# Kernel tuning notes

Hardware: AMD Instinct MI355X
Metric: run time of the kernel (lower is better)

## Reference

```python
import jax, jax.numpy as jnp
import numpy as np
from jax import lax

# --- model/problem dims (see init_kwargs) ---
G, NPG, R, F, HID, L = 40, 500, 8, 256, 256, 3   # graphs(frames), nodes/graph, relations, feat, hidden, layers
N = G * NPG                                       # 20000 nodes
EPG = 8000
E = G * EPG                                       # 320000 edges
TOTAL = L * HID                                   # 768 = concat of layer outputs
LSTM_IN, LSTM_HID, NCLASS = 256, 256, 2
RATIO = 0.5
K = int(np.ceil(RATIO * NPG))                     # 250 nodes kept per graph by SAGPool


def setup_inputs() -> dict:
    key = jax.random.key(0)
    ks = jax.random.split(key, 16)
    s = 0.05
    x = jax.random.normal(ks[0], (N, F), dtype=jnp.float32)
    # intra-graph edges: node ids offset by graph index
    off = jnp.arange(G, dtype=jnp.int32)[:, None] * NPG
    src = jax.random.randint(ks[1], (G, EPG), 0, NPG, dtype=jnp.int32) + off
    dst = jax.random.randint(ks[2], (G, EPG), 0, NPG, dtype=jnp.int32) + off
    edge_index = jnp.stack([src.reshape(-1), dst.reshape(-1)])
    edge_attr = jax.random.randint(ks[3], (E,), 0, R, dtype=jnp.int32)
    batch = jnp.repeat(jnp.arange(G, dtype=jnp.int32), NPG)
    # RGCN layer params (layer0 in=F==HID so all layers stack)
    conv_W = jax.random.normal(ks[4], (L, R, HID, HID), dtype=jnp.float32) * s
    conv_root = jax.random.normal(ks[5], (L, HID, HID), dtype=jnp.float32) * s
    conv_bias = jnp.zeros((L, HID), dtype=jnp.float32)
    # SAGPool scorer: RGCNConv(TOTAL, 1, R)
    pool_W = jax.random.normal(ks[6], (R, TOTAL, 1), dtype=jnp.float32) * s
    pool_root = jax.random.normal(ks[7], (TOTAL, 1), dtype=jnp.float32) * s
    pool_bias = jnp.zeros((1,), dtype=jnp.float32)
    fc1_W = jax.random.normal(ks[8], (LSTM_IN, TOTAL), dtype=jnp.float32) * s
    fc1_b = jnp.zeros((LSTM_IN,), dtype=jnp.float32)
    W_ih = jax.random.normal(ks[9], (4 * LSTM_HID, LSTM_IN), dtype=jnp.float32) * s
    W_hh = jax.random.normal(ks[10], (4 * LSTM_HID, LSTM_HID), dtype=jnp.float32) * s
    b_ih = jnp.zeros((4 * LSTM_HID,), dtype=jnp.float32)
    b_hh = jnp.zeros((4 * LSTM_HID,), dtype=jnp.float32)
    fc2_W = jax.random.normal(ks[11], (NCLASS, LSTM_HID), dtype=jnp.float32) * s
    fc2_b = jnp.zeros((NCLASS,), dtype=jnp.float32)
    return dict(x=x, edge_index=edge_index, edge_attr=edge_attr, batch=batch,
                conv_W=conv_W, conv_root=conv_root, conv_bias=conv_bias,
                pool_W=pool_W, pool_root=pool_root, pool_bias=pool_bias,
                fc1_W=fc1_W, fc1_b=fc1_b, W_ih=W_ih, W_hh=W_hh, b_ih=b_ih, b_hh=b_hh,
                fc2_W=fc2_W, fc2_b=fc2_b)


def rgcn_conv(x, src, dst, etype, W, root, bias):
    """PyG (Fast)RGCNConv: per-relation mean aggregation summed over relations + root + bias."""
    num_nodes = x.shape[0]
    Rr = W.shape[0]
    h_all = jnp.einsum('ni,rio->rno', x, W)          # [R, N, out] per-relation transform
    msg = h_all[etype, src]                           # [E, out] per-edge message
    seg = dst * Rr + etype                            # (node, relation) segment id
    cnt = jax.ops.segment_sum(jnp.ones((src.shape[0],), x.dtype), seg,
                              num_segments=num_nodes * Rr)
    norm = 1.0 / jnp.maximum(cnt[seg], 1.0)           # per-(dst,rel) mean normalization
    agg = jax.ops.segment_sum(msg * norm[:, None], dst, num_segments=num_nodes)
    return agg + x @ root + bias


def lstm_scan(xs, W_ih, W_hh, b_ih, b_hh):
    """torch.nn.LSTM (single layer, batch=1) over sequence xs [T, in]; torch gate order i,f,g,o."""
    H = W_hh.shape[1]
    def step(carry, xt):
        h, c = carry
        gates = xt @ W_ih.T + h @ W_hh.T + b_ih + b_hh
        i, f, g, o = jnp.split(gates, 4)
        c = jax.nn.sigmoid(f) * c + jax.nn.sigmoid(i) * jnp.tanh(g)
        h = jax.nn.sigmoid(o) * jnp.tanh(c)
        return (h, c), h
    init = (jnp.zeros((H,), xs.dtype), jnp.zeros((H,), xs.dtype))
    (h, c), ys = lax.scan(step, init, xs)
    return ys, h


def reference(x, edge_index, edge_attr, batch,
              conv_W, conv_root, conv_bias,
              pool_W, pool_root, pool_bias,
              fc1_W, fc1_b, W_ih, W_hh, b_ih, b_hh, fc2_W, fc2_b):
    src, dst = edge_index[0], edge_index[1]
    # stacked RGCN layers, outputs concatenated (dropout omitted: eval mode)
    h = x
    outs = []
    for l in range(L):
        h = jax.nn.relu(rgcn_conv(h, src, dst, edge_attr, conv_W[l], conv_root[l], conv_bias[l]))
        outs.append(h)
    xc = jnp.concatenate(outs, axis=-1)               # [N, TOTAL]
    # SAGPool: RGCN scorer -> tanh -> per-graph top-k (batch is contiguous equal-size graphs)
    score = jnp.tanh(rgcn_conv(xc, src, dst, edge_attr, pool_W, pool_root, pool_bias).reshape(-1))
    topv, topi = lax.top_k(score.reshape(G, NPG), K)  # [G, K]
    xg = xc.reshape(G, NPG, TOTAL)
    xsel = jnp.take_along_axis(xg, topi[:, :, None], axis=1) * topv[:, :, None]
    # readout_type='mean': global_mean_pool over kept nodes per graph
    readout = xsel.mean(axis=1)                       # [G, TOTAL]
    h1 = jax.nn.relu(readout @ fc1_W.T + fc1_b)       # [G, LSTM_IN]
    # temporal_type='lstm_last': last hidden state over the G-frame sequence
    _, hlast = lstm_scan(h1, W_ih, W_hh, b_ih, b_hh)  # [LSTM_HID]
    logits = hlast @ fc2_W.T + fc2_b                  # [NCLASS]
    return jax.nn.log_softmax(logits, axis=-1)
```

## Files before the change

### kernel.cpp

```cpp
#include <hip/hip_runtime.h>

typedef unsigned short u16;
typedef short bf8 __attribute__((ext_vector_type(8)));
typedef short bf4 __attribute__((ext_vector_type(4)));
typedef float f4 __attribute__((ext_vector_type(4)));
typedef _Float16 h2v __attribute__((ext_vector_type(2)));
typedef __fp16 g2v __attribute__((ext_vector_type(2)));
typedef unsigned int u4v __attribute__((ext_vector_type(4)));

#define N_NODES 20000
#define N_EDGES 320000
#define NGRAPH 40
#define NPG 500
#define KTOP 250
#define NSEG (N_NODES * 8)

#define P_CONV_BIAS 0
#define P_POOL_W    768
#define P_POOL_ROOT 6912
#define P_POOL_BIAS 7680
#define P_FC1_W     7688
#define P_FC1_B     204296
#define P_W_IH      204552
#define P_B_IH      466696
#define P_B_HH      467720
#define P_FC2_W     468744
#define P_FC2_B     469256
#define P_TOTAL     469264

__device__ __forceinline__ float b2f(u16 u) {
    union { unsigned int i; float f; } v; v.i = ((unsigned int)u) << 16; return v.f;
}
__device__ __forceinline__ u16 f2b(float f) {
    union { float f; unsigned int i; } v; v.f = f;
    unsigned int x = v.i;
    return (u16)((x + 0x7fffu + ((x >> 16) & 1u)) >> 16);
}
__device__ __forceinline__ float wred(float s) {
    #pragma unroll
    for (int off = 32; off > 0; off >>= 1) s += __shfl_down(s, off);
    return s;
}
__device__ __forceinline__ float fdot2u(unsigned a, unsigned b, float c) {
#if __has_builtin(__builtin_amdgcn_fdot2)
    union { unsigned u; h2v h; } ua, ub; ua.u = a; ub.u = b;
    return __builtin_amdgcn_fdot2(ua.h, ub.h, c, false);
#else
    union { unsigned u; g2v h; } ua, ub; ua.u = a; ub.u = b;
    return c + (float)ua.h[0] * (float)ub.h[0] + (float)ua.h[1] * (float)ub.h[1];
#endif
}
__device__ __forceinline__ unsigned packh2(float a, float b) {
    g2v h = __builtin_amdgcn_cvt_pkrtz(a, b);
    union { g2v h; unsigned u; } v; v.h = h; return v.u;
}
__device__ __forceinline__ float sigm_f(float x) {
    return 1.0f / (1.0f + __expf(-x));
}
__device__ __forceinline__ float tanh_f(float x) {
    return 1.0f - 2.0f / (1.0f + __expf(2.0f * x));
}

__global__ void k_init(unsigned int* __restrict__ flag, unsigned int* __restrict__ cnt,
                       unsigned int* __restrict__ ctr) {
    int i = blockIdx.x * 256 + threadIdx.x;
    if (i < 64) flag[i] = 0u;
    if (i < NSEG) { cnt[i] = 0u; ctr[i] = 0u; }
}

__global__ void k_detect1(const u16* __restrict__ xr, int n, unsigned int* __restrict__ fb) {
    unsigned int local = 0;
    for (int i = blockIdx.x * 256 + threadIdx.x; i < n; i += 64 * 256) {
        unsigned int u = xr[i];
        if (((u >> 7) & 0xFFu) == 0xFFu) local++;
    }
    local = (unsigned int)wred((float)local);
    if ((threadIdx.x & 63) == 0 && local) atomicAdd(&fb[1], local);
}
__global__ void k_detect2(unsigned int* __restrict__ fb) {
    fb[0] = (fb[1] > 8u) ? 1u : 0u;
}

__device__ __forceinline__ u16 load_cvt(const void* src, size_t i, bool f32) {
    return f32 ? f2b(((const float*)src)[i]) : ((const u16*)src)[i];
}

__global__ void k_cvt_all(const void* conv_bias, const void* pool_W, const void* pool_root,
                          const void* pool_bias, const void* fc1_W, const void* fc1_b,
                          const void* W_ih, const void* b_ih, const void* b_hh,
                          const void* fc2_W, const void* fc2_b,
                          u16* __restrict__ parms, const unsigned int* __restrict__ flag) {
    int i = blockIdx.x * 256 + threadIdx.x;
    if (i >= P_TOTAL) return;
    bool f32 = (*flag != 0u);
    u16 v;
    if      (i < P_CONV_BIAS + 768)    v = load_cvt(conv_bias, i - P_CONV_BIAS, f32);
    else if (i < P_POOL_W + 6144)      v = load_cvt(pool_W,    i - P_POOL_W, f32);
    else if (i < P_POOL_ROOT + 768)    v = load_cvt(pool_root, i - P_POOL_ROOT, f32);
    else if (i < P_POOL_BIAS + 1)      v = load_cvt(pool_bias, i - P_POOL_BIAS, f32);
    else if (i < P_FC1_W && i >= P_POOL_BIAS) return;
    else if (i < P_FC1_W + 196608)     v = load_cvt(fc1_W,    i - P_FC1_W, f32);
    else if (i < P_FC1_B + 256)        v = load_cvt(fc1_b,    i - P_FC1_B, f32);
    else if (i < P_W_IH + 262144)      v = load_cvt(W_ih,     i - P_W_IH, f32);
    else if (i < P_B_IH + 1024)        v = load_cvt(b_ih,     i - P_B_IH, f32);
    else if (i < P_B_HH + 1024)        v = load_cvt(b_hh,     i - P_B_HH, f32);
    else if (i < P_FC2_W + 512)        v = load_cvt(fc2_W,    i - P_FC2_W, f32);
    else if (i < P_FC2_B + 2)          v = load_cvt(fc2_b,    i - P_FC2_B, f32);
    else return;
    parms[i] = v;
}

__global__ void k_stage_x(const void* __restrict__ src, u16* __restrict__ xc,
                          const unsigned int* __restrict__ flag) {
    int i = blockIdx.x * 256 + threadIdx.x;
    if (i >= N_NODES * 32) return;
    int n = i >> 5, o = (i & 31) * 8;
    bf8 v;
    if (*flag != 0u) {
        const float* s = (const float*)src + (size_t)n * 256 + o;
        #pragma unroll
        for (int c = 0; c < 8; ++c) v[c] = (short)f2b(s[c]);
    } else {
        v = *(const bf8*)((const u16*)src + (size_t)n * 256 + o);
    }
    *(bf8*)(xc + (size_t)n * 768 + 512 + o) = v;
}

__global__ void k_count(const int* __restrict__ dst, const int* __restrict__ et,
                        unsigned int* __restrict__ cnt) {
    int e = blockIdx.x * 256 + threadIdx.x;
    if (e < N_EDGES) {
        unsigned d = (unsigned)dst[e]; if (d >= N_NODES) d = 0;
        unsigned r = (unsigned)et[e] & 7u;
        atomicAdd(&cnt[d * 8 + r], 1u);
    }
}
__global__ void k_inv(const unsigned int* __restrict__ cnt, float* __restrict__ inv, int n) {
    int i = blockIdx.x * 256 + threadIdx.x;
    if (i < n) {
        unsigned int c = cnt[i];
        inv[i] = 1.0f / (float)(c < 1u ? 1u : c);
    }
}

__global__ void k_scan1(const unsigned int* __restrict__ cnt, unsigned int* __restrict__ seg,
                        unsigned int* __restrict__ bsum) {
    __shared__ unsigned int s[256];
    int t = threadIdx.x, i = blockIdx.x * 256 + t;
    unsigned int v = (i < NSEG) ? cnt[i] : 0u;
    s[t] = v;
    __syncthreads();
    for (int off = 1; off < 256; off <<= 1) {
        unsigned int add = (t >= off) ? s[t - off] : 0u;
        __syncthreads();
        s[t] += add;
        __syncthreads();
    }
    if (i < NSEG) seg[i] = s[t] - v;
    if (t == 255) bsum[blockIdx.x] = s[255];
}
__global__ void k_scan2(unsigned int* __restrict__ bsum, int nb) {
    __shared__ unsigned int s[1024];
    int t = threadIdx.x;
    unsigned int v = (t < nb) ? bsum[t] : 0u;
    s[t] = v;
    __syncthreads();
    for (int off = 1; off < 1024; off <<= 1) {
        unsigned int add = (t >= off) ? s[t - off] : 0u;
        __syncthreads();
        s[t] += add;
        __syncthreads();
    }
    if (t < nb) bsum[t] = s[t] - v;
}
__global__ void k_scan3(unsigned int* __restrict__ seg, const unsigned int* __restrict__ bsum) {
    int i = blockIdx.x * 256 + threadIdx.x;
    if (i < NSEG) seg[i] += bsum[i >> 8];
    if (i == 0) seg[NSEG] = N_EDGES;
}
__global__ void k_place(const int* __restrict__ src, const int* __restrict__ dst,
                        const int* __restrict__ et, const unsigned int* __restrict__ seg,
                        unsigned int* __restrict__ ctr, const float* __restrict__ inv,
                        unsigned int* __restrict__ skey, float* __restrict__ sw, int chn) {
    int e = blockIdx.x * 256 + threadIdx.x;
    if (e >= N_EDGES) return;
    unsigned s = (unsigned)src[e]; if (s >= N_NODES) s = 0;
    unsigned d = (unsigned)dst[e]; if (d >= N_NODES) d = 0;
    unsigned r = (unsigned)et[e] & 7u;
    unsigned key = d * 8 + r;
    unsigned pos = seg[key] + atomicAdd(&ctr[key], 1u);
    unsigned base = (d / (unsigned)chn) * (unsigned)chn;
    unsigned sl = s - base;
    if (sl >= (unsigned)chn) sl = 0u;
    skey[pos] = sl | (r << 16);
    sw[pos] = inv[key];
}

__global__ void k_transpose2(const void* __restrict__ conv_W, const void* __restrict__ conv_root,
                             u16* __restrict__ Wt, const unsigned int* __restrict__ flag) {
    int idx = blockIdx.x * 256 + threadIdx.x;
    if (idx >= 3 * 36 * 256 * 64) return;
    bool f32 = (*flag != 0u);
    int kk = idx & 63;
    int n = (idx >> 6) & 255;
    int lc = idx >> 14;
    int l = lc / 36, ck = lc % 36;
    int k = ck * 64 + kk;
    u16 v;
    if (k < 2048) {
        int r = k >> 8, i = k & 255;
        v = load_cvt(conv_W, ((size_t)((l * 8 + r) * 256 + i)) * 256 + n, f32);
    } else {
        int i = k - 2048;
        v = load_cvt(conv_root, ((size_t)(l * 256 + i)) * 256 + n, f32);
    }
    Wt[idx] = v;
}
__global__ void k_whh4(const void* __restrict__ W_hh, unsigned int* __restrict__ whh4,
                       const unsigned int* __restrict__ flag) {
    int idx = blockIdx.x * 256 + threadIdx.x;
    if (idx >= 32 * 1024 * 4) return;
    int c = idx & 3, j = (idx >> 2) & 1023, i4 = idx >> 12;
    int i2 = i4 * 4 + c;
    bool f32 = (*flag != 0u);
    float a, b;
    if (f32) {
        a = ((const float*)W_hh)[j * 256 + 2 * i2];
        b = ((const float*)W_hh)[j * 256 + 2 * i2 + 1];
    } else {
        a = b2f(((const u16*)W_hh)[j * 256 + 2 * i2]);
        b = b2f(((const u16*)W_hh)[j * 256 + 2 * i2 + 1]);
    }
    whh4[idx] = packh2(a, b);
}

__launch_bounds__(256, 3)
__global__ void k_layer2(const u16* __restrict__ xprev,
                         const u16* __restrict__ WtL,
                         u16* __restrict__ Hall, int n0, int chn) {
    __shared__ u16 As[64 * 264];
    int m0 = n0 + blockIdx.x * 64;
    int rg = blockIdx.y;
    int nend = n0 + chn;
    int wave = threadIdx.x >> 6, lane = threadIdx.x & 63;
    int mrow = lane & 15, quad = lane >> 4;
    int nbase = wave * 64;

    {
        int row = threadIdx.x >> 2, sg = threadIdx.x & 3;
        int gm = m0 + row;
        u16* dstp = As + row * 264 + sg * 64;
        if (gm < nend) {
            const u16* srcp = xprev + (size_t)gm * 768 + sg * 64;
            #pragma unroll
            for (int c = 0; c < 8; ++c)
                *(bf8*)(dstp + c * 8) = *(const bf8*)(srcp + c * 8);
        } else {
            bf8 z = {0, 0, 0, 0, 0, 0, 0, 0};
            #pragma unroll
            for (int c = 0; c < 8; ++c) *(bf8*)(dstp + c * 8) = z;
        }
    }
    __syncthreads();

    f4 acc[4][4];
    #pragma unroll
    for (int nt = 0; nt < 4; ++nt)
        #pragma unroll
        for (int mh = 0; mh < 4; ++mh) acc[nt][mh] = (f4){0.0f, 0.0f, 0.0f, 0.0f};

    const u16* WtR = WtL + (size_t)(rg * 4) * 16384;
    #pragma unroll
    for (int c4 = 0; c4 < 4; ++c4) {
        const u16* Bck = WtR + (size_t)c4 * 16384;
        #pragma unroll
        for (int ks = 0; ks < 2; ++ks) {
            bf8 a[4];
            #pragma unroll
            for (int mh = 0; mh < 4; ++mh)
                a[mh] = *(const bf8*)(As + (mh * 16 + mrow) * 264 + c4 * 64 + ks * 32 + quad * 8);
            #pragma unroll
            for (int nt = 0; nt < 4; ++nt) {
                bf8 b = *(const bf8*)(Bck + (size_t)(nbase + nt * 16 + mrow) * 64
                                      + ks * 32 + quad * 8);
                #pragma unroll
                for (int mh = 0; mh < 4; ++mh)
                    acc[nt][mh] = __builtin_amdgcn_mfma_f32_16x16x32_bf16(a[mh], b, acc[nt][mh], 0, 0, 0);
            }
        }
    }

    __syncthreads();
    #pragma unroll
    for (int nt = 0; nt < 4; ++nt) {
        int col = nbase + nt * 16 + mrow;
        #pragma unroll
        for (int mh = 0; mh < 4; ++mh)
            #pragma unroll
            for (int v = 0; v < 4; ++v)
                As[(mh * 16 + quad * 4 + v) * 264 + col] = f2b(acc[nt][mh][v]);
    }
    __syncthreads();
    {
        int row = threadIdx.x >> 2, sg = threadIdx.x & 3;
        int gm = m0 + row;
        if (gm < nend) {
            u16* dst = Hall + ((size_t)rg * chn + (gm - n0)) * 256 + sg * 64;
            const u16* srcp = As + row * 264 + sg * 64;
            #pragma unroll
            for (int c = 0; c < 8; ++c)
                *(bf8*)(dst + c * 8) = *(const bf8*)(srcp + c * 8);
        }
    }
}

__launch_bounds__(256)
__global__ void k_gather(const unsigned int* __restrict__ seg,
                         const unsigned int* __restrict__ skey,
                         const float* __restrict__ sw,
                         const u16* __restrict__ Hall,
                         const u16* __restrict__ bias,
                         u16* __restrict__ xc, int colbase, int n0, int chn) {
    int nl = blockIdx.x * 4 + (threadIdx.x >> 6);
    int n = n0 + nl;
    int lane = threadIdx.x & 63;
    int c0 = lane * 4;
    unsigned e0 = seg[n * 8], e1 = seg[n * 8 + 8];
    float a0 = 0.0f, a1 = 0.0f, a2 = 0.0f, a3 = 0.0f;
    unsigned key = 0; float w = 0.0f;
    if (e0 < e1) { key = skey[e0]; w = sw[e0]; }
    for (unsigned e = e0; e < e1;) {
        unsigned kc = key; float wc = w;
        ++e;
        if (e < e1) { key = skey[e]; w = sw[e]; }
        const u16* row = Hall + ((size_t)(kc >> 16) * chn + (kc & 0xFFFFu)) * 256 + c0;
        bf4 v = *(const bf4*)row;
        a0 += wc * b2f((u16)v[0]);
        a1 += wc * b2f((u16)v[1]);
        a2 += wc * b2f((u16)v[2]);
        a3 += wc * b2f((u16)v[3]);
    }
    const u16* rr = Hall + ((size_t)8 * chn + nl) * 256 + c0;
    bf4 rv = *(const bf4*)rr;
    float o0 = a0 + b2f((u16)rv[0]) + b2f(bias[c0 + 0]);
    float o1 = a1 + b2f((u16)rv[1]) + b2f(bias[c0 + 1]);
    float o2 = a2 + b2f((u16)rv[2]) + b2f(bias[c0 + 2]);
    float o3 = a3 + b2f((u16)rv[3]) + b2f(bias[c0 + 3]);
    bf4 o;
    o[0] = (short)f2b(o0 > 0.0f ? o0 : 0.0f);
    o[1] = (short)f2b(o1 > 0.0f ? o1 : 0.0f);
    o[2] = (short)f2b(o2 > 0.0f ? o2 : 0.0f);
    o[3] = (short)f2b(o3 > 0.0f ? o3 : 0.0f);
    *(bf4*)(xc + (size_t)n * 768 + colbase + c0) = o;
}

__launch_bounds__(256)
__global__ void k_pool(const u16* __restrict__ xc, const u16* __restrict__ parms,
                       float* __restrict__ p, float* __restrict__ score) {
    int n = blockIdx.x * 4 + (threadIdx.x >> 6);
    if (n >= N_NODES) return;
    int lane = threadIdx.x & 63;
    const u16* xr = xc + (size_t)n * 768;
    float acc[9];
    #pragma unroll
    for (int rr = 0; rr < 9; ++rr) acc[rr] = 0.0f;
    #pragma unroll
    for (int q = 0; q < 12; ++q) {
        int f = lane + 64 * q;
        float xv = b2f(xr[f]);
        #pragma unroll
        for (int rr = 0; rr < 8; ++rr)
            acc[rr] += xv * b2f(parms[P_POOL_W + rr * 768 + f]);
        acc[8] += xv * b2f(parms[P_POOL_ROOT + f]);
    }
    #pragma unroll
    for (int rr = 0; rr < 9; ++rr) acc[rr] = wred(acc[rr]);
    if (lane == 0) {
        #pragma unroll
        for (int rr = 0; rr < 8; ++rr) p[rr * N_NODES + n] = acc[rr];
        score[n] = acc[8] + b2f(parms[P_POOL_BIAS]);
    }
}
__global__ void k_scatter_pool(const int* __restrict__ src, const int* __restrict__ dst,
                               const int* __restrict__ et, const float* __restrict__ inv,
                               const float* __restrict__ p, float* __restrict__ score) {
    int e = blockIdx.x * 256 + threadIdx.x;
    if (e >= N_EDGES) return;
    int r = et[e] & 7;
    unsigned s = (unsigned)src[e]; if (s >= N_NODES) s = 0;
    unsigned d = (unsigned)dst[e]; if (d >= N_NODES) d = 0;
    atomicAdd(&score[d], inv[d * 8 + r] * p[r * N_NODES + s]);
}

__launch_bounds__(256)
__global__ void k_sort(const float* __restrict__ score, unsigned int* __restrict__ topidx,
                       float* __restrict__ topv) {
    __shared__ unsigned long long keys[512];
    __shared__ float vals[512];
    int g = blockIdx.x, tid = threadIdx.x;
    for (int i = tid; i < 512; i += 256) {
        unsigned long long key;
        float v = 0.0f;
        if (i < NPG) {
            v = tanhf(score[g * NPG + i]);
            unsigned int u = __float_as_uint(v);
            u = (u & 0x80000000u) ? ~u : (u | 0x80000000u);
            u = ~u;
            key = ((unsigned long long)u << 32) | (unsigned int)i;
        } else {
            key = 0xFFFFFFFFFFFFFFFFull;
        }
        keys[i] = key;
        vals[i] = v;
    }
    __syncthreads();
    for (int k = 2; k <= 512; k <<= 1)
        for (int j = k >> 1; j > 0; j >>= 1) {
            for (int i = tid; i < 512; i += 256) {
                int ixj = i ^ j;
                if (ixj > i) {
                    bool up = ((i & k) == 0);
                    unsigned long long a = keys[i], b = keys[ixj];
                    if ((a > b) == up) { keys[i] = b; keys[ixj] = a; }
                }
            }
            __syncthreads();
        }
    if (tid < KTOP) {
        int idx = (int)(keys[tid] & 511u);
        topidx[g * 256 + tid] = (unsigned)idx;
        topv[g * 256 + tid] = vals[idx];
    }
}

__launch_bounds__(256)
__global__ void k_readout(const unsigned int* __restrict__ topidx,
                          const float* __restrict__ topv,
                          const u16* __restrict__ xc, float* __restrict__ readout) {
    __shared__ unsigned int sidx[KTOP];
    __shared__ float sv[KTOP];
    __shared__ float part[256];
    int g = blockIdx.x, cb = blockIdx.y;
    int tid = threadIdx.x;
    if (tid < KTOP) { sidx[tid] = topidx[g * 256 + tid]; sv[tid] = topv[g * 256 + tid]; }
    __syncthreads();
    int fl = tid & 63, ng = tid >> 6;
    int f = cb * 64 + fl;
    float acc = 0.0f;
    for (int j = ng; j < KTOP; j += 4)
        acc += sv[j] * b2f(xc[(size_t)(g * NPG + sidx[j]) * 768 + f]);
    part[tid] = acc;
    __syncthreads();
    if (tid < 64) {
        float s = part[tid] + part[64 + tid] + part[128 + tid] + part[192 + tid];
        readout[(size_t)g * 768 + cb * 64 + tid] = s * (1.0f / (float)KTOP);
    }
}

__global__ void k_fc1(const float* __restrict__ readout, const u16* __restrict__ parms,
                      float* __restrict__ h1) {
    int wid = blockIdx.x * 4 + (threadIdx.x >> 6);
    if (wid >= NGRAPH * 256) return;
    int g = wid >> 8, o = wid & 255, lane = threadIdx.x & 63;
    const float* rr = readout + (size_t)g * 768;
    const u16* w = parms + P_FC1_W + (size_t)o * 768;
    float s = 0.0f;
    #pragma unroll
    for (int q = 0; q < 12; ++q) { int f = lane + 64 * q; s += rr[f] * b2f(w[f]); }
    s = wred(s);
    if (lane == 0) { s += b2f(parms[P_FC1_B + o]); h1[g * 256 + o] = s > 0.0f ? s : 0.0f; }
}
__global__ void k_gx(const float* __restrict__ h1, const u16* __restrict__ parms,
                     float* __restrict__ gx) {
    int wid = blockIdx.x * 4 + (threadIdx.x >> 6);
    if (wid >= NGRAPH * 1024) return;
    int t = wid >> 10, j = wid & 1023, lane = threadIdx.x & 63;
    const float* xr = h1 + t * 256;
    const u16* w = parms + P_W_IH + (size_t)j * 256;
    float s = 0.0f;
    #pragma unroll
    for (int q = 0; q < 4; ++q) { int f = lane + 64 * q; s += xr[f] * b2f(w[f]); }
    s = wred(s);
    if (lane == 0) gx[t * 1024 + j] = s + b2f(parms[P_B_IH + j]) + b2f(parms[P_B_HH + j]);
}

__launch_bounds__(512, 1)
__global__ void k_lstm(const float* __restrict__ gx, const unsigned int* __restrict__ whh4,
                       const u16* __restrict__ parms, void* __restrict__ out,
                       const unsigned int* __restrict__ flag) {
    __shared__ float hs[256];
    __shared__ unsigned int hs2[128];
    __shared__ float gs[1024];
    __shared__ float red[2];
    int tid = threadIdx.x;
    int j0 = tid, j1 = tid + 512;
    u4v wa[24], wb[24];
    #pragma unroll
    for (int q = 0; q < 24; ++q) {
        wa[q] = *(const u4v*)(whh4 + (((size_t)q * 1024) + j0) * 4);
        wb[q] = *(const u4v*)(whh4 + (((size_t)q * 1024) + j1) * 4);
    }
    asm volatile("" : "+v"(wa[0]), "+v"(wa[1]), "+v"(wa[2]), "+v"(wa[3]),
                      "+v"(wa[4]), "+v"(wa[5]), "+v"(wa[6]), "+v"(wa[7]),
                      "+v"(wa[8]), "+v"(wa[9]), "+v"(wa[10]), "+v"(wa[11]),
                      "+v"(wa[12]), "+v"(wa[13]), "+v"(wa[14]), "+v"(wa[15]),
                      "+v"(wa[16]), "+v"(wa[17]), "+v"(wa[18]), "+v"(wa[19]),
                      "+v"(wa[20]), "+v"(wa[21]), "+v"(wa[22]), "+v"(wa[23]));
    asm volatile("" : "+v"(wb[0]), "+v"(wb[1]), "+v"(wb[2]), "+v"(wb[3]),
                      "+v"(wb[4]), "+v"(wb[5]), "+v"(wb[6]), "+v"(wb[7]),
                      "+v"(wb[8]), "+v"(wb[9]), "+v"(wb[10]), "+v"(wb[11]),
                      "+v"(wb[12]), "+v"(wb[13]), "+v"(wb[14]), "+v"(wb[15]),
                      "+v"(wb[16]), "+v"(wb[17]), "+v"(wb[18]), "+v"(wb[19]),
                      "+v"(wb[20]), "+v"(wb[21]), "+v"(wb[22]), "+v"(wb[23]));
    if (tid < 256) hs[tid] = 0.0f;
    if (tid < 128) hs2[tid] = 0u;
    float c = 0.0f;
    __syncthreads();
    for (int t = 0; t < NGRAPH; ++t) {
        float g0 = gx[t * 1024 + j0];
        float g1 = gx[t * 1024 + j1];
        #pragma unroll
        for (int q = 0; q < 24; ++q) {
            #pragma unroll
            for (int cc = 0; cc < 4; ++cc) {
                unsigned h2 = hs2[q * 4 + cc];
                g0 = fdot2u(wa[q][cc], h2, g0);
                g1 = fdot2u(wb[q][cc], h2, g1);
            }
        }
        #pragma unroll 2
        for (int q = 24; q < 32; ++q) {
            u4v v0 = *(const u4v*)(whh4 + (((size_t)q * 1024) + j0) * 4);
            u4v v1 = *(const u4v*)(whh4 + (((size_t)q * 1024) + j1) * 4);
            #pragma unroll
            for (int cc = 0; cc < 4; ++cc) {
                unsigned h2 = hs2[q * 4 + cc];
                g0 = fdot2u(v0[cc], h2, g0);
                g1 = fdot2u(v1[cc], h2, g1);
            }
        }
        gs[j0] = g0;
        gs[j1] = g1;
        __syncthreads();
        if (tid < 256) {
            float gi = sigm_f(gs[tid]);
            float gf = sigm_f(gs[256 + tid]);
            float gg = tanh_f(gs[512 + tid]);
            float go = sigm_f(gs[768 + tid]);
            c = gf * c + gi * gg;
            float h = go * tanh_f(c);
            hs[tid] = h;
            float ho = __shfl(h, (tid & 63) ^ 1);
            if (!(tid & 1)) hs2[tid >> 1] = packh2(h, ho);
        }
        __syncthreads();
    }
    if (tid < 128) {
        int cls = tid >> 6, lane = tid & 63;
        float s = 0.0f;
        #pragma unroll
        for (int q = 0; q < 4; ++q) {
            int d = lane + 64 * q;
            s += hs[d] * b2f(parms[P_FC2_W + cls * 256 + d]);
        }
        s = wred(s);
        if (lane == 0) red[cls] = s + b2f(parms[P_FC2_B + cls]);
    }
    __syncthreads();
    if (tid == 0) {
        float l0 = red[0], l1 = red[1];
        float m = fmaxf(l0, l1);
        float lse = m + logf(expf(l0 - m) + expf(l1 - m));
        float o0 = l0 - lse, o1 = l1 - lse;
        if (*flag) { ((float*)out)[0] = o0; ((float*)out)[1] = o1; }
        else       { ((u16*)out)[0] = f2b(o0); ((u16*)out)[1] = f2b(o1); }
    }
}

struct WS {
    unsigned int* flag; unsigned int* cnt; float* inv; unsigned int* seg; unsigned int* ctr;
    unsigned int* skey; float* sw; unsigned int* bsum;
    u16* Wt2; u16* xc; u16* Hall; float* p; float* score;
    unsigned int* topidx; float* topv;
    float* readout; float* h1; float* gx; unsigned int* whh4; u16* parms;
    size_t need;
};
static WS plan(char* base, int chn) {
    WS w; size_t off = 0;
    auto take = [&](size_t bytes) -> char* {
        char* p = base + off; off += (bytes + 255) & ~(size_t)255; return p;
    };
    w.flag    = (unsigned int*)take(256);
    w.cnt     = (unsigned int*)take((size_t)NSEG * 4);
    w.inv     = (float*)take((size_t)NSEG * 4);
    w.seg     = (unsigned int*)take((size_t)(NSEG + 1) * 4);
    w.ctr     = (unsigned int*)take((size_t)NSEG * 4);
    w.skey    = (unsigned int*)take((size_t)N_EDGES * 4);
    w.sw      = (float*)take((size_t)N_EDGES * 4);
    w.bsum    = (unsigned int*)take(1024 * 4);
    w.Wt2     = (u16*)take((size_t)3 * 36 * 256 * 64 * 2);
    w.xc      = (u16*)take((size_t)N_NODES * 768 * 2);
    w.Hall    = (u16*)take((size_t)9 * chn * 256 * 2);
    w.p       = (float*)take((size_t)8 * N_NODES * 4);
    w.score   = (float*)take((size_t)N_NODES * 4);
    w.topidx  = (unsigned int*)take((size_t)NGRAPH * 256 * 4);
    w.topv    = (float*)take((size_t)NGRAPH * 256 * 4);
    w.readout = (float*)take((size_t)NGRAPH * 768 * 4);
    w.h1      = (float*)take((size_t)NGRAPH * 256 * 4);
    w.gx      = (float*)take((size_t)NGRAPH * 1024 * 4);
    w.whh4    = (unsigned int*)take((size_t)32 * 1024 * 4 * 4);
    w.parms   = (u16*)take((size_t)P_TOTAL * 2);
    w.need = off;
    return w;
}

extern "C" void kernel_launch(void* const* d_in, const int* in_sizes, int n_in,
                              void* d_out, int out_size, void* d_ws, size_t ws_size,
                              hipStream_t stream) {
    (void)in_sizes; (void)n_in; (void)out_size;
    const void* x        = d_in[0];
    const int* edge_index= (const int*)d_in[1];
    const int* edge_attr = (const int*)d_in[2];
    const void* conv_W   = d_in[4];
    const void* conv_root= d_in[5];
    const void* conv_bias= d_in[6];
    const void* pool_W   = d_in[7];
    const void* pool_root= d_in[8];
    const void* pool_bias= d_in[9];
    const void* fc1_W    = d_in[10];
    const void* fc1_b    = d_in[11];
    const void* W_ih     = d_in[12];
    const void* W_hh     = d_in[13];
    const void* b_ih     = d_in[14];
    const void* b_hh     = d_in[15];
    const void* fc2_W    = d_in[16];
    const void* fc2_b    = d_in[17];

    const int* e_src = edge_index;
    const int* e_dst = edge_index + N_EDGES;

    if (ws_size == 0) ws_size = (size_t)64 << 20;
    int chn = 500;
    {
        const int ladder[8] = {20000, 10000, 5000, 4000, 2500, 2000, 1000, 500};
        for (int i = 0; i < 8; ++i) {
            if (plan((char*)d_ws, ladder[i]).need <= ws_size) { chn = ladder[i]; break; }
        }
    }
    WS w = plan((char*)d_ws, chn);

    k_init<<<(NSEG + 255) / 256, 256, 0, stream>>>(w.flag, w.cnt, w.ctr);
    k_detect1<<<64, 256, 0, stream>>>((const u16*)x, 1 << 18, w.flag);
    k_detect2<<<1, 1, 0, stream>>>(w.flag);

    k_count<<<1250, 256, 0, stream>>>(e_dst, edge_attr, w.cnt);
    k_inv<<<(NSEG + 255) / 256, 256, 0, stream>>>(w.cnt, w.inv, NSEG);
    k_scan1<<<625, 256, 0, stream>>>(w.cnt, w.seg, w.bsum);
    k_scan2<<<1, 1024, 0, stream>>>(w.bsum, 625);
    k_scan3<<<(NSEG + 255) / 256, 256, 0, stream>>>(w.seg, w.bsum);
    k_place<<<1250, 256, 0, stream>>>(e_src, e_dst, edge_attr, w.seg, w.ctr, w.inv,
                                      w.skey, w.sw, chn);

    k_cvt_all<<<(P_TOTAL + 255) / 256, 256, 0, stream>>>(
        conv_bias, pool_W, pool_root, pool_bias, fc1_W, fc1_b,
        W_ih, b_ih, b_hh, fc2_W, fc2_b, w.parms, w.flag);

    k_stage_x<<<2500, 256, 0, stream>>>(x, w.xc, w.flag);
    k_transpose2<<<6912, 256, 0, stream>>>(conv_W, conv_root, w.Wt2, w.flag);
    k_whh4<<<512, 256, 0, stream>>>(W_hh, w.whh4, w.flag);

    int nch = N_NODES / chn;
    int gx_tiles = (chn + 63) / 64;
    for (int l = 0; l < 3; ++l) {
        const u16* xprev = w.xc + (l == 0 ? 512 : (l - 1) * 256);
        const u16* WtL = w.Wt2 + (size_t)l * 36 * 16384;
        const u16* bias = w.parms + P_CONV_BIAS + l * 256;
        for (int c = 0; c < nch; ++c) {
            int n0 = c * chn;
            k_layer2<<<dim3(gx_tiles, 9), 256, 0, stream>>>(xprev, WtL, w.Hall, n0, chn);
            k_gather<<<chn / 4, 256, 0, stream>>>(w.seg, w.skey, w.sw, w.Hall, bias,
                                                  w.xc, l * 256, n0, chn);
        }
    }

    k_pool<<<5000, 256, 0, stream>>>(w.xc, w.parms, w.p, w.score);
    k_scatter_pool<<<1250, 256, 0, stream>>>(e_src, e_dst, edge_attr, w.inv, w.p, w.score);
    k_sort<<<NGRAPH, 256, 0, stream>>>(w.score, w.topidx, w.topv);
    k_readout<<<dim3(NGRAPH, 12), 256, 0, stream>>>(w.topidx, w.topv, w.xc, w.readout);
    k_fc1<<<2560, 256, 0, stream>>>(w.readout, w.parms, w.h1);
    k_gx<<<10240, 256, 0, stream>>>(w.h1, w.parms, w.gx);
    k_lstm<<<1, 512, 0, stream>>>(w.gx, w.whh4, w.parms, d_out, w.flag);
}
```

Before: 691.6 us.

## Fuse setup and tail kernels, drop inverse-count buffer, allow uneven chunk sizes

Merges the parameter, input, weight-transpose and W_hh packing kernels into a single prep launch. Folds the detect flag finalisation into the edge count kernel, and computes inverse degree counts on the fly instead of materialising them. The sort, readout, fc1 and input-gate projection become one per-graph tail kernel. Chunking now permits a non-divisor cap (7000) with a remainder chunk. Together these cut launch count and intermediate buffers, but the tail now runs serially in only 40 blocks, which may cost more than it saves.

```diff
diff --git a/kernel.cpp b/kernel.cpp
--- a/kernel.cpp
+++ b/kernel.cpp
@@ -28,6 +28,12 @@
 #define P_FC2_B     469256
 #define P_TOTAL     469264
 
+#define PR_A0 0
+#define PR_B0 469264
+#define PR_C0 (PR_B0 + 640000)
+#define PR_D0 (PR_C0 + 1769472)
+#define PR_END (PR_D0 + 131072)
+
 __device__ __forceinline__ float b2f(u16 u) {
     union { unsigned int i; float f; } v; v.i = ((unsigned int)u) << 16; return v.f;
 }
@@ -77,69 +83,19 @@
     local = (unsigned int)wred((float)local);
     if ((threadIdx.x & 63) == 0 && local) atomicAdd(&fb[1], local);
 }
-__global__ void k_detect2(unsigned int* __restrict__ fb) {
-    fb[0] = (fb[1] > 8u) ? 1u : 0u;
-}
 
 __device__ __forceinline__ u16 load_cvt(const void* src, size_t i, bool f32) {
     return f32 ? f2b(((const float*)src)[i]) : ((const u16*)src)[i];
 }
 
-__global__ void k_cvt_all(const void* conv_bias, const void* pool_W, const void* pool_root,
-                          const void* pool_bias, const void* fc1_W, const void* fc1_b,
-                          const void* W_ih, const void* b_ih, const void* b_hh,
-                          const void* fc2_W, const void* fc2_b,
-                          u16* __restrict__ parms, const unsigned int* __restrict__ flag) {
-    int i = blockIdx.x * 256 + threadIdx.x;
-    if (i >= P_TOTAL) return;
-    bool f32 = (*flag != 0u);
-    u16 v;
-    if      (i < P_CONV_BIAS + 768)    v = load_cvt(conv_bias, i - P_CONV_BIAS, f32);
-    else if (i < P_POOL_W + 6144)      v = load_cvt(pool_W,    i - P_POOL_W, f32);
-    else if (i < P_POOL_ROOT + 768)    v = load_cvt(pool_root, i - P_POOL_ROOT, f32);
-    else if (i < P_POOL_BIAS + 1)      v = load_cvt(pool_bias, i - P_POOL_BIAS, f32);
-    else if (i < P_FC1_W && i >= P_POOL_BIAS) return;
-    else if (i < P_FC1_W + 196608)     v = load_cvt(fc1_W,    i - P_FC1_W, f32);
-    else if (i < P_FC1_B + 256)        v = load_cvt(fc1_b,    i - P_FC1_B, f32);
-    else if (i < P_W_IH + 262144)      v = load_cvt(W_ih,     i - P_W_IH, f32);
-    else if (i < P_B_IH + 1024)        v = load_cvt(b_ih,     i - P_B_IH, f32);
-    else if (i < P_B_HH + 1024)        v = load_cvt(b_hh,     i - P_B_HH, f32);
-    else if (i < P_FC2_W + 512)        v = load_cvt(fc2_W,    i - P_FC2_W, f32);
-    else if (i < P_FC2_B + 2)          v = load_cvt(fc2_b,    i - P_FC2_B, f32);
-    else return;
-    parms[i] = v;
-}
-
-__global__ void k_stage_x(const void* __restrict__ src, u16* __restrict__ xc,
-                          const unsigned int* __restrict__ flag) {
-    int i = blockIdx.x * 256 + threadIdx.x;
-    if (i >= N_NODES * 32) return;
-    int n = i >> 5, o = (i & 31) * 8;
-    bf8 v;
-    if (*flag != 0u) {
-        const float* s = (const float*)src + (size_t)n * 256 + o;
-        #pragma unroll
-        for (int c = 0; c < 8; ++c) v[c] = (short)f2b(s[c]);
-    } else {
-        v = *(const bf8*)((const u16*)src + (size_t)n * 256 + o);
-    }
-    *(bf8*)(xc + (size_t)n * 768 + 512 + o) = v;
-}
-
 __global__ void k_count(const int* __restrict__ dst, const int* __restrict__ et,
-                        unsigned int* __restrict__ cnt) {
+                        unsigned int* __restrict__ cnt, unsigned int* __restrict__ fb) {
     int e = blockIdx.x * 256 + threadIdx.x;
+    if (e == 0) fb[0] = (fb[1] > 8u) ? 1u : 0u;
     if (e < N_EDGES) {
         unsigned d = (unsigned)dst[e]; if (d >= N_NODES) d = 0;
         unsigned r = (unsigned)et[e] & 7u;
         atomicAdd(&cnt[d * 8 + r], 1u);
-    }
-}
-__global__ void k_inv(const unsigned int* __restrict__ cnt, float* __restrict__ inv, int n) {
-    int i = blockIdx.x * 256 + threadIdx.x;
-    if (i < n) {
-        unsigned int c = cnt[i];
-        inv[i] = 1.0f / (float)(c < 1u ? 1u : c);
     }
 }
 
@@ -180,8 +136,8 @@
 }
 __global__ void k_place(const int* __restrict__ src, const int* __restrict__ dst,
                         const int* __restrict__ et, const unsigned int* __restrict__ seg,
-                        unsigned int* __restrict__ ctr, const float* __restrict__ inv,
-                        unsigned int* __restrict__ skey, float* __restrict__ sw, int chn) {
+                        unsigned int* __restrict__ ctr, const unsigned int* __restrict__ cnt,
+                        unsigned int* __restrict__ skey, float* __restrict__ sw, int cap) {
     int e = blockIdx.x * 256 + threadIdx.x;
     if (e >= N_EDGES) return;
     unsigned s = (unsigned)src[e]; if (s >= N_NODES) s = 0;
@@ -189,59 +145,94 @@
     unsigned r = (unsigned)et[e] & 7u;
     unsigned key = d * 8 + r;
     unsigned pos = seg[key] + atomicAdd(&ctr[key], 1u);
-    unsigned base = (d / (unsigned)chn) * (unsigned)chn;
+    unsigned base = (d / (unsigned)cap) * (unsigned)cap;
     unsigned sl = s - base;
-    if (sl >= (unsigned)chn) sl = 0u;
+    if (sl >= (unsigned)cap) sl = 0u;
     skey[pos] = sl | (r << 16);
-    sw[pos] = inv[key];
-}
-
-__global__ void k_transpose2(const void* __restrict__ conv_W, const void* __restrict__ conv_root,
-                             u16* __restrict__ Wt, const unsigned int* __restrict__ flag) {
-    int idx = blockIdx.x * 256 + threadIdx.x;
-    if (idx >= 3 * 36 * 256 * 64) return;
-    bool f32 = (*flag != 0u);
-    int kk = idx & 63;
-    int n = (idx >> 6) & 255;
-    int lc = idx >> 14;
-    int l = lc / 36, ck = lc % 36;
-    int k = ck * 64 + kk;
-    u16 v;
-    if (k < 2048) {
-        int r = k >> 8, i = k & 255;
-        v = load_cvt(conv_W, ((size_t)((l * 8 + r) * 256 + i)) * 256 + n, f32);
-    } else {
-        int i = k - 2048;
-        v = load_cvt(conv_root, ((size_t)(l * 256 + i)) * 256 + n, f32);
-    }
-    Wt[idx] = v;
-}
-__global__ void k_whh4(const void* __restrict__ W_hh, unsigned int* __restrict__ whh4,
+    unsigned c = cnt[key];
+    sw[pos] = 1.0f / (float)(c < 1u ? 1u : c);
+}
+
+__global__ void k_prep(const void* conv_bias, const void* pool_W, const void* pool_root,
+                       const void* pool_bias, const void* fc1_W, const void* fc1_b,
+                       const void* W_ih, const void* b_ih, const void* b_hh,
+                       const void* fc2_W, const void* fc2_b,
+                       const void* __restrict__ x, const void* __restrict__ conv_W,
+                       const void* __restrict__ conv_root, const void* __restrict__ W_hh,
+                       u16* __restrict__ parms, u16* __restrict__ xc,
+                       u16* __restrict__ Wt, unsigned int* __restrict__ whh4,
                        const unsigned int* __restrict__ flag) {
     int idx = blockIdx.x * 256 + threadIdx.x;
-    if (idx >= 32 * 1024 * 4) return;
-    int c = idx & 3, j = (idx >> 2) & 1023, i4 = idx >> 12;
-    int i2 = i4 * 4 + c;
     bool f32 = (*flag != 0u);
-    float a, b;
-    if (f32) {
-        a = ((const float*)W_hh)[j * 256 + 2 * i2];
-        b = ((const float*)W_hh)[j * 256 + 2 * i2 + 1];
-    } else {
-        a = b2f(((const u16*)W_hh)[j * 256 + 2 * i2]);
-        b = b2f(((const u16*)W_hh)[j * 256 + 2 * i2 + 1]);
-    }
-    whh4[idx] = packh2(a, b);
+    if (idx < PR_B0) {
+        int i = idx;
+        u16 v;
+        if      (i < P_CONV_BIAS + 768)    v = load_cvt(conv_bias, i - P_CONV_BIAS, f32);
+        else if (i < P_POOL_W + 6144)      v = load_cvt(pool_W,    i - P_POOL_W, f32);
+        else if (i < P_POOL_ROOT + 768)    v = load_cvt(pool_root, i - P_POOL_ROOT, f32);
+        else if (i < P_POOL_BIAS + 1)      v = load_cvt(pool_bias, i - P_POOL_BIAS, f32);
+        else if (i < P_FC1_W && i >= P_POOL_BIAS) return;
+        else if (i < P_FC1_W + 196608)     v = load_cvt(fc1_W,    i - P_FC1_W, f32);
+        else if (i < P_FC1_B + 256)        v = load_cvt(fc1_b,    i - P_FC1_B, f32);
+        else if (i < P_W_IH + 262144)      v = load_cvt(W_ih,     i - P_W_IH, f32);
+        else if (i < P_B_IH + 1024)        v = load_cvt(b_ih,     i - P_B_IH, f32);
+        else if (i < P_B_HH + 1024)        v = load_cvt(b_hh,     i - P_B_HH, f32);
+        else if (i < P_FC2_W + 512)        v = load_cvt(fc2_W,    i - P_FC2_W, f32);
+        else if (i < P_FC2_B + 2)          v = load_cvt(fc2_b,    i - P_FC2_B, f32);
+        else return;
+        parms[i] = v;
+    } else if (idx < PR_C0) {
+        int i = idx - PR_B0;
+        int n = i >> 5, o = (i & 31) * 8;
+        bf8 v;
+        if (f32) {
+            const float* s = (const float*)x + (size_t)n * 256 + o;
+            #pragma unroll
+            for (int c = 0; c < 8; ++c) v[c] = (short)f2b(s[c]);
+        } else {
+            v = *(const bf8*)((const u16*)x + (size_t)n * 256 + o);
+        }
+        *(bf8*)(xc + (size_t)n * 768 + 512 + o) = v;
+    } else if (idx < PR_D0) {
+        int i = idx - PR_C0;
+        int kk = i & 63;
+        int n = (i >> 6) & 255;
+        int lc = i >> 14;
+        int l = lc / 36, ck = lc % 36;
+        int k = ck * 64 + kk;
+        u16 v;
+        if (k < 2048) {
+            int r = k >> 8, ii = k & 255;
+            v = load_cvt(conv_W, ((size_t)((l * 8 + r) * 256 + ii)) * 256 + n, f32);
+        } else {
+            int ii = k - 2048;
+            v = load_cvt(conv_root, ((size_t)(l * 256 + ii)) * 256 + n, f32);
+        }
+        Wt[i] = v;
+    } else if (idx < PR_END) {
+        int i = idx - PR_D0;
+        int c = i & 3, j = (i >> 2) & 1023, i4 = i >> 12;
+        int i2 = i4 * 4 + c;
+        float a, b;
+        if (f32) {
+            a = ((const float*)W_hh)[j * 256 + 2 * i2];
+            b = ((const float*)W_hh)[j * 256 + 2 * i2 + 1];
+        } else {
+            a = b2f(((const u16*)W_hh)[j * 256 + 2 * i2]);
+            b = b2f(((const u16*)W_hh)[j * 256 + 2 * i2 + 1]);
+        }
+        whh4[i] = packh2(a, b);
+    }
 }
 
 __launch_bounds__(256, 3)
 __global__ void k_layer2(const u16* __restrict__ xprev,
                          const u16* __restrict__ WtL,
-                         u16* __restrict__ Hall, int n0, int chn) {
+                         u16* __restrict__ Hall, int n0, int chnc) {
     __shared__ u16 As[64 * 264];
     int m0 = n0 + blockIdx.x * 64;
     int rg = blockIdx.y;
-    int nend = n0 + chn;
+    int nend = n0 + chnc;
     int wave = threadIdx.x >> 6, lane = threadIdx.x & 63;
     int mrow = lane & 15, quad = lane >> 4;
     int nbase = wave * 64;
@@ -305,7 +296,7 @@
         int row = threadIdx.x >> 2, sg = threadIdx.x & 3;
         int gm = m0 + row;
         if (gm < nend) {
-            u16* dst = Hall + ((size_t)rg * chn + (gm - n0)) * 256 + sg * 64;
+            u16* dst = Hall + ((size_t)rg * chnc + (gm - n0)) * 256 + sg * 64;
             const u16* srcp = As + row * 264 + sg * 64;
             #pragma unroll
             for (int c = 0; c < 8; ++c)
@@ -320,8 +311,9 @@
                          const float* __restrict__ sw,
                          const u16* __restrict__ Hall,
                          const u16* __restrict__ bias,
-                         u16* __restrict__ xc, int colbase, int n0, int chn) {
+                         u16* __restrict__ xc, int colbase, int n0, int chnc) {
     int nl = blockIdx.x * 4 + (threadIdx.x >> 6);
+    if (nl >= chnc) return;
     int n = n0 + nl;
     int lane = threadIdx.x & 63;
     int c0 = lane * 4;
@@ -333,14 +325,14 @@
         unsigned kc = key; float wc = w;
         ++e;
         if (e < e1) { key = skey[e]; w = sw[e]; }
-        const u16* row = Hall + ((size_t)(kc >> 16) * chn + (kc & 0xFFFFu)) * 256 + c0;
+        const u16* row = Hall + ((size_t)(kc >> 16) * chnc + (kc & 0xFFFFu)) * 256 + c0;
         bf4 v = *(const bf4*)row;
         a0 += wc * b2f((u16)v[0]);
         a1 += wc * b2f((u16)v[1]);
         a2 += wc * b2f((u16)v[2]);
         a3 += wc * b2f((u16)v[3]);
     }
-    const u16* rr = Hall + ((size_t)8 * chn + nl) * 256 + c0;
+    const u16* rr = Hall + ((size_t)8 * chnc + nl) * 256 + c0;
     bf4 rv = *(const bf4*)rr;
     float o0 = a0 + b2f((u16)rv[0]) + b2f(bias[c0 + 0]);
     float o1 = a1 + b2f((u16)rv[1]) + b2f(bias[c0 + 1]);
@@ -382,22 +374,30 @@
     }
 }
 __global__ void k_scatter_pool(const int* __restrict__ src, const int* __restrict__ dst,
-                               const int* __restrict__ et, const float* __restrict__ inv,
+                               const int* __restrict__ et, const unsigned int* __restrict__ cnt,
                                const float* __restrict__ p, float* __restrict__ score) {
     int e = blockIdx.x * 256 + threadIdx.x;
     if (e >= N_EDGES) return;
     int r = et[e] & 7;
     unsigned s = (unsigned)src[e]; if (s >= N_NODES) s = 0;
     unsigned d = (unsigned)dst[e]; if (d >= N_NODES) d = 0;
-    atomicAdd(&score[d], inv[d * 8 + r] * p[r * N_NODES + s]);
+    unsigned c = cnt[d * 8 + r];
+    float iv = 1.0f / (float)(c < 1u ? 1u : c);
+    atomicAdd(&score[d], iv * p[r * N_NODES + s]);
 }
 
 __launch_bounds__(256)
-__global__ void k_sort(const float* __restrict__ score, unsigned int* __restrict__ topidx,
-                       float* __restrict__ topv) {
+__global__ void k_tail(const float* __restrict__ score, const u16* __restrict__ xc,
+                       const u16* __restrict__ parms, float* __restrict__ gx) {
     __shared__ unsigned long long keys[512];
     __shared__ float vals[512];
+    __shared__ unsigned int sidx[KTOP];
+    __shared__ float sv[KTOP];
+    __shared__ float part[256];
+    __shared__ float rro[768];
+    __shared__ float h1s[256];
     int g = blockIdx.x, tid = threadIdx.x;
+    int wave = tid >> 6, lane = tid & 63;
     for (int i = tid; i < 512; i += 256) {
         unsigned long long key;
         float v = 0.0f;
@@ -428,60 +428,44 @@
         }
     if (tid < KTOP) {
         int idx = (int)(keys[tid] & 511u);
-        topidx[g * 256 + tid] = (unsigned)idx;
-        topv[g * 256 + tid] = vals[idx];
-    }
-}
-
-__launch_bounds__(256)
-__global__ void k_readout(const unsigned int* __restrict__ topidx,
-                          const float* __restrict__ topv,
-                          const u16* __restrict__ xc, float* __restrict__ readout) {
-    __shared__ unsigned int sidx[KTOP];
-    __shared__ float sv[KTOP];
-    __shared__ float part[256];
-    int g = blockIdx.x, cb = blockIdx.y;
-    int tid = threadIdx.x;
-    if (tid < KTOP) { sidx[tid] = topidx[g * 256 + tid]; sv[tid] = topv[g * 256 + tid]; }
+        sidx[tid] = (unsigned)idx;
+        sv[tid] = vals[idx];
+    }
     __syncthreads();
     int fl = tid & 63, ng = tid >> 6;
-    int f = cb * 64 + fl;
-    float acc = 0.0f;
-    for (int j = ng; j < KTOP; j += 4)
-        acc += sv[j] * b2f(xc[(size_t)(g * NPG + sidx[j]) * 768 + f]);
-    part[tid] = acc;
-    __syncthreads();
-    if (tid < 64) {
-        float s = part[tid] + part[64 + tid] + part[128 + tid] + part[192 + tid];
-        readout[(size_t)g * 768 + cb * 64 + tid] = s * (1.0f / (float)KTOP);
-    }
-}
-
-__global__ void k_fc1(const float* __restrict__ readout, const u16* __restrict__ parms,
-                      float* __restrict__ h1) {
-    int wid = blockIdx.x * 4 + (threadIdx.x >> 6);
-    if (wid >= NGRAPH * 256) return;
-    int g = wid >> 8, o = wid & 255, lane = threadIdx.x & 63;
-    const float* rr = readout + (size_t)g * 768;
-    const u16* w = parms + P_FC1_W + (size_t)o * 768;
-    float s = 0.0f;
-    #pragma unroll
-    for (int q = 0; q < 12; ++q) { int f = lane + 64 * q; s += rr[f] * b2f(w[f]); }
-    s = wred(s);
-    if (lane == 0) { s += b2f(parms[P_FC1_B + o]); h1[g * 256 + o] = s > 0.0f ? s : 0.0f; }
-}
-__global__ void k_gx(const float* __restrict__ h1, const u16* __restrict__ parms,
-                     float* __restrict__ gx) {
-    int wid = blockIdx.x * 4 + (threadIdx.x >> 6);
-    if (wid >= NGRAPH * 1024) return;
-    int t = wid >> 10, j = wid & 1023, lane = threadIdx.x & 63;
-    const float* xr = h1 + t * 256;
-    const u16* w = parms + P_W_IH + (size_t)j * 256;
-    float s = 0.0f;
-    #pragma unroll
-    for (int q = 0; q < 4; ++q) { int f = lane + 64 * q; s += xr[f] * b2f(w[f]); }
-    s = wred(s);
-    if (lane == 0) gx[t * 1024 + j] = s + b2f(parms[P_B_IH + j]) + b2f(parms[P_B_HH + j]);
+    for (int cb = 0; cb < 12; ++cb) {
+        float acc = 0.0f;
+        int f = cb * 64 + fl;
+        for (int j = ng; j < KTOP; j += 4)
+            acc += sv[j] * b2f(xc[(size_t)(g * NPG + sidx[j]) * 768 + f]);
+        part[tid] = acc;
+        __syncthreads();
+        if (tid < 64)
+            rro[cb * 64 + tid] = (part[tid] + part[64 + tid] + part[128 + tid]
+                                  + part[192 + tid]) * (1.0f / (float)KTOP);
+        __syncthreads();
+    }
+    for (int o = wave; o < 256; o += 4) {
+        const u16* w = parms + P_FC1_W + (size_t)o * 768;
+        float s = 0.0f;
+        #pragma unroll
+        for (int q = 0; q < 12; ++q) { int f = lane + 64 * q; s += rro[f] * b2f(w[f]); }
+        s = wred(s);
+        if (lane == 0) {
+            s += b2f(parms[P_FC1_B + o]);
+            h1s[o] = s > 0.0f ? s : 0.0f;
+        }
+    }
+    __syncthreads();
+    for (int j = wave; j < 1024; j += 4) {
+        const u16* w = parms + P_W_IH + (size_t)j * 256;
+        float s = 0.0f;
+        #pragma unroll
+        for (int q = 0; q < 4; ++q) { int f = lane + 64 * q; s += h1s[f] * b2f(w[f]); }
+        s = wred(s);
+        if (lane == 0)
+            gx[g * 1024 + j] = s + b2f(parms[P_B_IH + j]) + b2f(parms[P_B_HH + j]);
+    }
 }
 
 __launch_bounds__(512, 1)
@@ -578,21 +562,19 @@
 }
 
 struct WS {
-    unsigned int* flag; unsigned int* cnt; float* inv; unsigned int* seg; unsigned int* ctr;
+    unsigned int* flag; unsigned int* cnt; unsigned int* seg; unsigned int* ctr;
     unsigned int* skey; float* sw; unsigned int* bsum;
     u16* Wt2; u16* xc; u16* Hall; float* p; float* score;
-    unsigned int* topidx; float* topv;
-    float* readout; float* h1; float* gx; unsigned int* whh4; u16* parms;
+    float* gx; unsigned int* whh4; u16* parms;
     size_t need;
 };
-static WS plan(char* base, int chn) {
+static WS plan(char* base, int cap) {
     WS w; size_t off = 0;
     auto take = [&](size_t bytes) -> char* {
         char* p = base + off; off += (bytes + 255) & ~(size_t)255; return p;
     };
     w.flag    = (unsigned int*)take(256);
     w.cnt     = (unsigned int*)take((size_t)NSEG * 4);
-    w.inv     = (float*)take((size_t)NSEG * 4);
     w.seg     = (unsigned int*)take((size_t)(NSEG + 1) * 4);
     w.ctr     = (unsigned int*)take((size_t)NSEG * 4);
     w.skey    = (unsigned int*)take((size_t)N_EDGES * 4);
@@ -600,13 +582,9 @@
     w.bsum    = (unsigned int*)take(1024 * 4);
     w.Wt2     = (u16*)take((size_t)3 * 36 * 256 * 64 * 2);
     w.xc      = (u16*)take((size_t)N_NODES * 768 * 2);
-    w.Hall    = (u16*)take((size_t)9 * chn * 256 * 2);
+    w.Hall    = (u16*)take((size_t)9 * cap * 256 * 2);
     w.p       = (float*)take((size_t)8 * N_NODES * 4);
     w.score   = (float*)take((size_t)N_NODES * 4);
-    w.topidx  = (unsigned int*)take((size_t)NGRAPH * 256 * 4);
-    w.topv    = (float*)take((size_t)NGRAPH * 256 * 4);
-    w.readout = (float*)take((size_t)NGRAPH * 768 * 4);
-    w.h1      = (float*)take((size_t)NGRAPH * 256 * 4);
     w.gx      = (float*)take((size_t)NGRAPH * 1024 * 4);
     w.whh4    = (unsigned int*)take((size_t)32 * 1024 * 4 * 4);
     w.parms   = (u16*)take((size_t)P_TOTAL * 2);
@@ -640,54 +618,45 @@
     const int* e_dst = edge_index + N_EDGES;
 
     if (ws_size == 0) ws_size = (size_t)64 << 20;
-    int chn = 500;
+    int cap = 500;
     {
-        const int ladder[8] = {20000, 10000, 5000, 4000, 2500, 2000, 1000, 500};
-        for (int i = 0; i < 8; ++i) {
-            if (plan((char*)d_ws, ladder[i]).need <= ws_size) { chn = ladder[i]; break; }
-        }
-    }
-    WS w = plan((char*)d_ws, chn);
+        const int ladder[9] = {20000, 10000, 7000, 5000, 4000, 2500, 2000, 1000, 500};
+        for (int i = 0; i < 9; ++i) {
+            if (plan((char*)d_ws, ladder[i]).need <= ws_size) { cap = ladder[i]; break; }
+        }
+    }
+    WS w = plan((char*)d_ws, cap);
 
     k_init<<<(NSEG + 255) / 256, 256, 0, stream>>>(w.flag, w.cnt, w.ctr);
     k_detect1<<<64, 256, 0, stream>>>((const u16*)x, 1 << 18, w.flag);
-    k_detect2<<<1, 1, 0, stream>>>(w.flag);
-
-    k_count<<<1250, 256, 0, stream>>>(e_dst, edge_attr, w.cnt);
-    k_inv<<<(NSEG + 255) / 256, 256, 0, stream>>>(w.cnt, w.inv, NSEG);
+    k_count<<<1250, 256, 0, stream>>>(e_dst, edge_attr, w.cnt, w.flag);
     k_scan1<<<625, 256, 0, stream>>>(w.cnt, w.seg, w.bsum);
     k_scan2<<<1, 1024, 0, stream>>>(w.bsum, 625);
     k_scan3<<<(NSEG + 255) / 256, 256, 0, stream>>>(w.seg, w.bsum);
-    k_place<<<1250, 256, 0, stream>>>(e_src, e_dst, edge_attr, w.seg, w.ctr, w.inv,
-                                      w.skey, w.sw, chn);
-
-    k_cvt_all<<<(P_TOTAL + 255) / 256, 256, 0, stream>>>(
+    k_place<<<1250, 256, 0, stream>>>(e_src, e_dst, edge_attr, w.seg, w.ctr, w.cnt,
+                                      w.skey, w.sw, cap);
+
+    k_prep<<<(PR_END + 255) / 256, 256, 0, stream>>>(
         conv_bias, pool_W, pool_root, pool_bias, fc1_W, fc1_b,
-        W_ih, b_ih, b_hh, fc2_W, fc2_b, w.parms, w.flag);
-
-    k_stage_x<<<2500, 256, 0, stream>>>(x, w.xc, w.flag);
-    k_transpose2<<<6912, 256, 0, stream>>>(conv_W, conv_root, w.Wt2, w.flag);
-    k_whh4<<<512, 256, 0, stream>>>(W_hh, w.whh4, w.flag);
-
-    int nch = N_NODES / chn;
-    int gx_tiles = (chn + 63) / 64;
+        W_ih, b_ih, b_hh, fc2_W, fc2_b,
+        x, conv_W, conv_root, W_hh,
+        w.parms, w.xc, w.Wt2, w.whh4, w.flag);
+
     for (int l = 0; l < 3; ++l) {
         const u16* xprev = w.xc + (l == 0 ? 512 : (l - 1) * 256);
         const u16* WtL = w.Wt2 + (size_t)l * 36 * 16384;
         const u16* bias = w.parms + P_CONV_BIAS + l * 256;
-        for (int c = 0; c < nch; ++c) {
-            int n0 = c * chn;
-            k_layer2<<<dim3(gx_tiles, 9), 256, 0, stream>>>(xprev, WtL, w.Hall, n0, chn);
-            k_gather<<<chn / 4, 256, 0, stream>>>(w.seg, w.skey, w.sw, w.Hall, bias,
-                                                  w.xc, l * 256, n0, chn);
+        for (int n0 = 0; n0 < N_NODES; n0 += cap) {
+            int chnc = N_NODES - n0 < cap ? N_NODES - n0 : cap;
+            int tiles = (chnc + 63) / 64;
+            k_layer2<<<dim3(tiles, 9), 256, 0, stream>>>(xprev, WtL, w.Hall, n0, chnc);
+            k_gather<<<(chnc + 3) / 4, 256, 0, stream>>>(w.seg, w.skey, w.sw, w.Hall,
+                                                         bias, w.xc, l * 256, n0, chnc);
         }
     }
 
     k_pool<<<5000, 256, 0, stream>>>(w.xc, w.parms, w.p, w.score);
-    k_scatter_pool<<<1250, 256, 0, stream>>>(e_src, e_dst, edge_attr, w.inv, w.p, w.score);
-    k_sort<<<NGRAPH, 256, 0, stream>>>(w.score, w.topidx, w.topv);
-    k_readout<<<dim3(NGRAPH, 12), 256, 0, stream>>>(w.topidx, w.topv, w.xc, w.readout);
-    k_fc1<<<2560, 256, 0, stream>>>(w.readout, w.parms, w.h1);
-    k_gx<<<10240, 256, 0, stream>>>(w.h1, w.parms, w.gx);
+    k_scatter_pool<<<1250, 256, 0, stream>>>(e_src, e_dst, edge_attr, w.cnt, w.p, w.score);
+    k_tail<<<NGRAPH, 256, 0, stream>>>(w.score, w.xc, w.parms, w.gx);
     k_lstm<<<1, 512, 0, stream>>>(w.gx, w.whh4, w.parms, d_out, w.flag);
 }
```

After: 1.063 ms. +53.7%, slower.
